# Kernel tuning notes

Hardware: AMD Instinct MI355X
Metric: run time of the kernel (lower is better)

## Reference

```python
import jax, jax.numpy as jnp
from jax import lax
import numpy as np

T_LOW, T_HIGH = 100.0, 200.0  # module defaults
H_IMG, W_IMG = 2048, 2048


def setup_inputs() -> dict:
    key = jax.random.key(0)
    x = jax.random.uniform(key, (H_IMG, W_IMG), dtype=jnp.float32)  # image in [0,1]
    return {"x": x}


def _sh(p, dy, dx, H, W):
    # shifted view of a 1-pixel-padded array
    return p[1 + dy:1 + dy + H, 1 + dx:1 + dx + W]


def _canny(x):
    H, W = x.shape
    # (x*255).astype(uint8): quantize (floor), values assumed in [0,1]
    img = jnp.clip(jnp.floor(x * 255.0), 0.0, 255.0)

    # --- 3x3 Sobel gradients, replicate border (cv2 default) ---
    p = jnp.pad(img, 1, mode='edge')
    s = lambda dy, dx: _sh(p, dy, dx, H, W)
    gx = (s(-1, 1) + 2.0 * s(0, 1) + s(1, 1)) - (s(-1, -1) + 2.0 * s(0, -1) + s(1, -1))
    gy = (s(1, -1) + 2.0 * s(1, 0) + s(1, 1)) - (s(-1, -1) + 2.0 * s(-1, 0) + s(-1, 1))
    mag = jnp.abs(gx) + jnp.abs(gy)  # L1 gradient magnitude (cv2 L2gradient=False)

    # --- non-maximum suppression along quantized gradient direction ---
    ang = jnp.mod(jnp.degrees(jnp.arctan2(gy, gx)), 180.0)
    mp = jnp.pad(mag, 1)  # zero-pad: out-of-image neighbors have magnitude 0
    n = lambda dy, dx: _sh(mp, dy, dx, H, W)
    d0 = (ang < 22.5) | (ang >= 157.5)            # ~0 deg   -> compare L/R
    d1 = (ang >= 22.5) & (ang < 67.5)             # ~45 deg  -> compare diag
    d2 = (ang >= 67.5) & (ang < 112.5)            # ~90 deg  -> compare U/D
    # remaining (~135 deg)                         -> other diag
    n1 = jnp.where(d0, n(0, 1), jnp.where(d1, n(-1, 1), jnp.where(d2, n(-1, 0), n(-1, -1))))
    n2 = jnp.where(d0, n(0, -1), jnp.where(d1, n(1, -1), jnp.where(d2, n(1, 0), n(1, 1))))
    keep = (mag >= n1) & (mag > n2)
    # border pixels are never edges (cv2 behavior)
    interior = jnp.zeros((H, W), bool).at[1:-1, 1:-1].set(True)
    keep = keep & interior

    # --- double threshold + hysteresis edge linking (8-connected) ---
    strong = lax.stop_gradient(keep & (mag > T_HIGH))
    weak = lax.stop_gradient(keep & (mag > T_LOW))

    def dilate8(m):
        mp2 = jnp.pad(m, 1)
        out = jnp.zeros_like(m)
        for dy in (-1, 0, 1):
            for dx in (-1, 0, 1):
                out = out | _sh(mp2, dy, dx, H, W)
        return out

    def body(c):
        cur, _ = c
        new = cur | (weak & dilate8(cur))
        return new, jnp.any(new != cur)

    edges, _ = lax.while_loop(lambda c: c[1], body, (strong, jnp.array(True)))

    # ToTensor() maps uint8 255 -> 1.0; expand to 3 channels
    e = edges.astype(jnp.float32)
    return jnp.broadcast_to(e[None], (3, H, W))


def reference(x):
    return _canny(x)
```

## Files before the change

### kernel.cpp

```cpp
#include <hip/hip_runtime.h>
#include <hip/hip_cooperative_groups.h>

namespace cg = cooperative_groups;

#define HH 2048
#define WW 2048
#define WPR 32
#define NPIX (HH * WW)
#define NWORDS (HH * WPR)

typedef unsigned long long u64;
typedef unsigned int u32;

__device__ inline int findRoot(int* __restrict__ f, int i) {
    int p = __hip_atomic_load(&f[i], __ATOMIC_RELAXED, __HIP_MEMORY_SCOPE_AGENT);
    while (p != i) {
        int gp = __hip_atomic_load(&f[p], __ATOMIC_RELAXED, __HIP_MEMORY_SCOPE_AGENT);
        if (gp != p)
            __hip_atomic_store(&f[i], gp, __ATOMIC_RELAXED, __HIP_MEMORY_SCOPE_AGENT);
        i = p; p = gp;
    }
    return i;
}

__device__ inline void unite(int* __restrict__ f, int a, int b) {
    int ra = findRoot(f, a), rb = findRoot(f, b);
    while (ra != rb) {
        if (ra > rb) { int t = ra; ra = rb; rb = t; }
        int old = atomicCAS(&f[rb], rb, ra);
        if (old == rb || old == ra) return;
        rb = findRoot(f, old);
    }
}

__device__ inline int findRootRO(const int* __restrict__ f, int i) {
    int p = __hip_atomic_load(&f[i], __ATOMIC_RELAXED, __HIP_MEMORY_SCOPE_AGENT);
    while (true) {
        int gp = __hip_atomic_load(&f[p], __ATOMIC_RELAXED, __HIP_MEMORY_SCOPE_AGENT);
        if (gp == p) return p;
        p = gp;
    }
}

__device__ inline int findRootL(volatile int* fl, int i) {
    int p = fl[i];
    while (p != i) {
        int gp = fl[p];
        if (gp != p) fl[i] = gp;
        i = p; p = gp;
    }
    return i;
}

__device__ inline void uniteL(int* fl, int a, int b) {
    int ra = findRootL(fl, a), rb = findRootL(fl, b);
    while (ra != rb) {
        if (ra > rb) { int t = ra; ra = rb; rb = t; }
        int old = atomicCAS(&fl[rb], rb, ra);
        if (old == rb || old == ra) return;
        rb = findRootL(fl, old);
    }
}

__device__ inline int dirClass(int gxv, int gyv) {
    int ay = gyv, ax = gxv;
    if (ay < 0) { ay = -ay; ax = -ax; }
    if (ay == 0) return 0;
    if (ax > 0) {
        int s = ay + ax, q = 2 * ax * ax;
        if (s * s < q) return 0;
        int t = ay - ax;
        return (t < 0 || t * t < q) ? 1 : 2;
    }
    if (ax == 0) return 2;
    int h = -ax, s = ay + h, q = 2 * h * h;
    if (s * s < q) return 0;
    int t = ay - h;
    return (t > 0 && t * t > q) ? 2 : 3;
}

__global__ __launch_bounds__(512) void canny_tile(
    const float* __restrict__ x, u64* __restrict__ weakG,
    u64* __restrict__ edgeBits, u64* __restrict__ pendBits, int* __restrict__ f)
{
    __shared__ int imgS[68 * 68];
    __shared__ unsigned short magS[66 * 66];
    __shared__ u64 wRow[64], sRow[64];
    __shared__ unsigned char touched[4097];
    int* fl = imgS;

    const int tid = threadIdx.x;
    const int x0 = blockIdx.x * 64;
    const int y0 = blockIdx.y * 64;

    for (int idx = tid; idx < 68 * 68; idx += 512) {
        int r = idx / 68, c = idx - r * 68;
        int gy = y0 - 2 + r; gy = gy < 0 ? 0 : (gy > HH - 1 ? HH - 1 : gy);
        int gx = x0 - 2 + c; gx = gx < 0 ? 0 : (gx > WW - 1 ? WW - 1 : gx);
        float v = floorf(x[gy * WW + gx] * 255.0f);
        v = fminf(fmaxf(v, 0.0f), 255.0f);
        imgS[idx] = (int)v;
    }
    __syncthreads();

    for (int idx = tid; idx < 66 * 66; idx += 512) {
        int r = idx / 66, c = idx - r * 66;
        int i0 = r * 68 + c;
        int a00 = imgS[i0],       a01 = imgS[i0 + 1],   a02 = imgS[i0 + 2];
        int a10 = imgS[i0 + 68],                        a12 = imgS[i0 + 70];
        int a20 = imgS[i0 + 136], a21 = imgS[i0 + 137], a22 = imgS[i0 + 138];
        int gxv = (a02 + 2 * a12 + a22) - (a00 + 2 * a10 + a20);
        int gyv = (a20 + 2 * a21 + a22) - (a00 + 2 * a01 + a02);
        int mag = abs(gxv) + abs(gyv);
        int cls = dirClass(gxv, gyv);
        magS[idx] = (unsigned short)((cls << 12) | mag);
    }
    __syncthreads();

    const int lane = tid & 63;
    const int wv = tid >> 6;
    for (int i = 0; i < 8; ++i) {
        int rr = wv * 8 + i;
        int gyp = y0 + rr;
        int mc = (rr + 1) * 66 + lane + 1;
        int mv = magS[mc];
        int cls = mv >> 12;
        int mag = mv & 0xFFF;
        int d1 = (cls == 0) ? -1 : 64 + cls;
        int n1 = magS[mc - d1] & 0xFFF;
        int n2 = magS[mc + d1] & 0xFFF;
        bool keep = (mag >= n1) && (mag > n2) && (gyp > 0) && (gyp < HH - 1);
        bool weak = keep && (mag > 100);
        bool strong = keep && (mag > 200);
        u64 ww = __ballot(weak);
        u64 sw = __ballot(strong);
        if (lane == 0) {
            u64 m = ~0ull;
            if (x0 == 0) m &= ~1ull;
            if (x0 + 64 == WW) m &= ~(1ull << 63);
            wRow[rr] = ww & m;
            sRow[rr] = sw & m;
        }
    }
    for (int i = tid; i < 4097; i += 512) { fl[i] = i; touched[i] = 0; }
    __syncthreads();

    {
        const int r = tid >> 3, o = tid & 7;
        const u64 omask = 0xFFull << (o * 8);
        const u64 w = wRow[r];
        const u64 above = r ? wRow[r - 1] : 0;
        const int base = r * 64 + 1;
        u64 m;
        m = (w & (w >> 1)) & omask;
        while (m) { int b = __builtin_ctzll(m); m &= m - 1; uniteL(fl, base + b, base + b + 1); }
        m = (w & above) & omask;
        while (m) { int b = __builtin_ctzll(m); m &= m - 1; uniteL(fl, base + b, base - 64 + b); }
        m = (w & (above << 1)) & omask;
        while (m) { int b = __builtin_ctzll(m); m &= m - 1; uniteL(fl, base + b, base - 64 + b - 1); }
        m = (w & (above >> 1)) & omask;
        while (m) { int b = __builtin_ctzll(m); m &= m - 1; uniteL(fl, base + b, base - 64 + b + 1); }
        m = sRow[r] & omask;
        while (m) { int b = __builtin_ctzll(m); m &= m - 1; uniteL(fl, 0, base + b); }
    }
    __syncthreads();

    if (tid < 256) {
        int grp = tid >> 6;
        int ln = tid & 63;
        int node = -1;
        if (grp == 0)      { if ((wRow[0]  >> ln) & 1ull) node = ln + 1; }
        else if (grp == 1) { if ((wRow[63] >> ln) & 1ull) node = 63 * 64 + ln + 1; }
        else if (grp == 2) { if (wRow[ln] & 1ull)         node = ln * 64 + 1; }
        else               { if (wRow[ln] >> 63)          node = ln * 64 + 63 + 1; }
        if (node > 0) touched[findRootL(fl, node)] = 1;
    }
    __syncthreads();

    for (int k = 0; k < 8; ++k) {
        int i = k * 512 + tid;
        int rr = i >> 6, cc = i & 63;
        int g = (y0 + rr) * WW + x0 + cc;
        int val = g;
        bool edge = false, pend = false;
        if ((wRow[rr] >> cc) & 1ull) {
            int rt = findRootL(fl, i + 1);
            if (rt == 0) { edge = true; val = 0; }
            else {
                val = (y0 + ((rt - 1) >> 6)) * WW + x0 + ((rt - 1) & 63);
                pend = touched[rt] != 0;
            }
        }
        f[g] = val;
        u64 eb = __ballot(edge);
        u64 pb = __ballot(pend);
        if (lane == 0) {
            int widx = (y0 + rr) * WPR + (x0 >> 6);
            edgeBits[widx] = eb;
            pendBits[widx] = pb;
        }
    }
    if (tid < 64) weakG[(y0 + tid) * WPR + blockIdx.x] = wRow[tid];
}

__global__ __launch_bounds__(256) void canny_boundary(
    const u64* __restrict__ weakG, int* __restrict__ f)
{
    int t = blockIdx.x * 256 + threadIdx.x;
    if (t < 65536) {
        int y = t >> 5, c = t & 31;
        if (c == 31) return;
        u64 w0 = weakG[y * WPR + c];
        u64 w1 = weakG[y * WPR + c + 1];
        int a = (int)(w0 >> 63) & 1, b = (int)w1 & 1;
        if (!(a | b)) return;
        int p63 = y * WW + c * 64 + 63;
        int p64 = p63 + 1;
        if (a & b) unite(f, p63, p64);
        if (y < HH - 1) {
            u64 w0d = weakG[(y + 1) * WPR + c];
            u64 w1d = weakG[(y + 1) * WPR + c + 1];
            if (a && (w1d & 1ull)) unite(f, p63, p64 + WW);
            if (b && (w0d >> 63)) unite(f, p64, p63 + WW);
        }
    } else {
        int idx = t - 65536;
        if (idx >= 31 * 2048) return;
        int y = 63 + (idx >> 11) * 64;
        int xx = idx & 2047;
        u64 w = weakG[y * WPR + (xx >> 6)];
        if (!((w >> (xx & 63)) & 1ull)) return;
        int p = y * WW + xx;
        u64 wd = weakG[(y + 1) * WPR + (xx >> 6)];
        if ((wd >> (xx & 63)) & 1ull) unite(f, p, p + WW);
        if (xx > 0) {
            u64 wl = weakG[(y + 1) * WPR + ((xx - 1) >> 6)];
            if ((wl >> ((xx - 1) & 63)) & 1ull) unite(f, p, p + WW - 1);
        }
        if (xx < WW - 1) {
            u64 wr = weakG[(y + 1) * WPR + ((xx + 1) >> 6)];
            if ((wr >> ((xx + 1) & 63)) & 1ull) unite(f, p, p + WW + 1);
        }
    }
}

__global__ __launch_bounds__(256) void canny_edgefuse(
    const u64* __restrict__ edgeBits, const u64* __restrict__ pendBits,
    const int* __restrict__ f, float* __restrict__ out)
{
    __shared__ unsigned short eS[256];
    const int tid = threadIdx.x;
    const int B = blockIdx.x * 4096;
    const int px0 = B + tid * 16;
    u64 ew = edgeBits[px0 >> 6];
    u64 pw = pendBits[px0 >> 6];
    const int sh = px0 & 63;
    u32 be = (u32)(ew >> sh) & 0xFFFFu;
    u32 bp = (u32)(pw >> sh) & 0xFFFFu;
    if (bp) {
        int lastp = -1, laste = 0;
        do {
            int b = __builtin_ctz(bp); bp &= bp - 1;
            int v = __hip_atomic_load(&f[px0 + b], __ATOMIC_RELAXED, __HIP_MEMORY_SCOPE_AGENT);
            int ed;
            if (v == 0) ed = 1;
            else if (v == px0 + b) ed = 0;
            else if (v == lastp) ed = laste;
            else { ed = (findRootRO(f, v) == 0); lastp = v; laste = ed; }
            be |= (u32)ed << b;
        } while (bp);
    }
    eS[tid] = (unsigned short)be;
    __syncthreads();

    #pragma unroll
    for (int ch = 0; ch < 3; ++ch) {
        #pragma unroll
        for (int j = 0; j < 4; ++j) {
            int idx = j * 256 + tid;
            u32 eb = (u32)(eS[idx >> 2] >> ((idx & 3) * 4)) & 0xFu;
            float4 v;
            v.x = (float)(eb & 1u);
            v.y = (float)((eb >> 1) & 1u);
            v.z = (float)((eb >> 2) & 1u);
            v.w = (float)((eb >> 3) & 1u);
            *reinterpret_cast<float4*>(out + (size_t)ch * NPIX + B + idx * 4) = v;
        }
    }
}

__global__ __launch_bounds__(256) void canny_prep(
    const float* __restrict__ x, u64* __restrict__ weakG,
    u64* __restrict__ strongG, unsigned int* __restrict__ flags)
{
    __shared__ int imgS[20][68];
    __shared__ int magS[18][68];
    const int tid = threadIdx.x;
    const int tx0 = blockIdx.x * 64;
    const int ty0 = blockIdx.y * 16;

    if (flags && blockIdx.x == 0 && blockIdx.y == 0 && tid < 2) flags[tid] = 0u;

    for (int idx = tid; idx < 20 * 68; idx += 256) {
        int r = idx / 68, c = idx - r * 68;
        int gy = ty0 - 2 + r; gy = gy < 0 ? 0 : (gy > HH - 1 ? HH - 1 : gy);
        int gx = tx0 - 2 + c; gx = gx < 0 ? 0 : (gx > WW - 1 ? WW - 1 : gx);
        float v = floorf(x[gy * WW + gx] * 255.0f);
        v = fminf(fmaxf(v, 0.0f), 255.0f);
        imgS[r][c] = (int)v;
    }
    __syncthreads();

    for (int idx = tid; idx < 18 * 66; idx += 256) {
        int r = idx / 66, c = idx - r * 66;
        int a00 = imgS[r][c],     a01 = imgS[r][c + 1],     a02 = imgS[r][c + 2];
        int a10 = imgS[r + 1][c],                           a12 = imgS[r + 1][c + 2];
        int a20 = imgS[r + 2][c], a21 = imgS[r + 2][c + 1], a22 = imgS[r + 2][c + 2];
        int gxv = (a02 + 2 * a12 + a22) - (a00 + 2 * a10 + a20);
        int gyv = (a20 + 2 * a21 + a22) - (a00 + 2 * a01 + a02);
        magS[r][c] = abs(gxv) + abs(gyv);
    }
    __syncthreads();

    const int lane = tid & 63;
    const int wv = tid >> 6;
    for (int i = 0; i < 4; ++i) {
        int rr = wv * 4 + i;
        int gyp = ty0 + rr;
        int r = rr + 1, c = lane + 1;
        int a00 = imgS[rr + 1][lane + 1], a01 = imgS[rr + 1][lane + 2], a02 = imgS[rr + 1][lane + 3];
        int a10 = imgS[rr + 2][lane + 1],                               a12 = imgS[rr + 2][lane + 3];
        int a20 = imgS[rr + 3][lane + 1], a21 = imgS[rr + 3][lane + 2], a22 = imgS[rr + 3][lane + 3];
        int gxv = (a02 + 2 * a12 + a22) - (a00 + 2 * a10 + a20);
        int gyv = (a20 + 2 * a21 + a22) - (a00 + 2 * a01 + a02);
        int mag = magS[r][c];
        int cls = dirClass(gxv, gyv);
        int n1, n2;
        if (cls == 0)      { n1 = magS[r][c + 1];     n2 = magS[r][c - 1]; }
        else if (cls == 1) { n1 = magS[r - 1][c + 1]; n2 = magS[r + 1][c - 1]; }
        else if (cls == 2) { n1 = magS[r - 1][c];     n2 = magS[r + 1][c]; }
        else               { n1 = magS[r - 1][c - 1]; n2 = magS[r + 1][c + 1]; }

        bool keep = (mag >= n1) && (mag > n2) && (gyp > 0) && (gyp < HH - 1);
        bool weak = keep && (mag > 100);
        bool strong = keep && (mag > 200);
        u64 ww = __ballot(weak);
        u64 sw = __ballot(strong);
        if (lane == 0) {
            u64 mm = ~0ull;
            if (tx0 == 0) mm &= ~1ull;
            if (tx0 + 64 == WW) mm &= ~(1ull << 63);
            int widx = gyp * WPR + (tx0 >> 6);
            weakG[widx] = ww & mm;
            strongG[widx] = sw & mm;
        }
    }
}

__global__ __launch_bounds__(256) void canny_hyst(
    const u64* __restrict__ weakG, u64* __restrict__ edgeG,
    unsigned int* __restrict__ flags, float* __restrict__ out)
{
    cg::grid_group grid = cg::this_grid();
    const int tid = threadIdx.x;
    const int b = blockIdx.x;
    const int r = tid >> 5;
    const int c = tid & 31;
    const int row0 = b * 8;
    __shared__ u64 weakL[8][32];
    __shared__ u64 edgeL[10][32];
    __shared__ int sChg[2];
    __shared__ int sAny;

    weakL[r][c] = weakG[(row0 + r) * WPR + c];
    edgeL[r + 1][c] = edgeG[(row0 + r) * WPR + c];

    int iter = 0;
    for (;;) {
        if (tid < 32) {
            u64 v = 0;
            if (b > 0) v = __hip_atomic_load(&edgeG[(row0 - 1) * WPR + tid],
                                             __ATOMIC_RELAXED, __HIP_MEMORY_SCOPE_AGENT);
            edgeL[0][tid] = v;
        } else if (tid < 64) {
            int cc = tid - 32;
            u64 v = 0;
            if (b < (int)gridDim.x - 1)
                v = __hip_atomic_load(&edgeG[(row0 + 8) * WPR + cc],
                                      __ATOMIC_RELAXED, __HIP_MEMORY_SCOPE_AGENT);
            edgeL[9][cc] = v;
        }
        if (tid == 0) sAny = 0;
        if (tid < 2) sChg[tid] = 0;
        __syncthreads();

        int p = 0;
        for (;;) {
            u64 up = edgeL[r][c],     upl = c ? edgeL[r][c - 1] : 0,     upr = (c < 31) ? edgeL[r][c + 1] : 0;
            u64 mi = edgeL[r + 1][c], mil = c ? edgeL[r + 1][c - 1] : 0, mir = (c < 31) ? edgeL[r + 1][c + 1] : 0;
            u64 dn = edgeL[r + 2][c], dnl = c ? edgeL[r + 2][c - 1] : 0, dnr = (c < 31) ? edgeL[r + 2][c + 1] : 0;
            u64 A = up | (up << 1) | (up >> 1) | (upl >> 63) | (upr << 63);
            u64 B = mi | (mi << 1) | (mi >> 1) | (mil >> 63) | (mir << 63);
            u64 C = dn | (dn << 1) | (dn >> 1) | (dnl >> 63) | (dnr << 63);
            u64 ne = mi | (weakL[r][c] & (A | B | C));
            bool chg = (ne != mi);
            __syncthreads();
            edgeL[r + 1][c] = ne;
            if (chg) { sChg[p] = 1; sAny = 1; }
            if (tid == 0) sChg[p ^ 1] = 0;
            __syncthreads();
            if (!sChg[p]) break;
            p ^= 1;
        }

        if (sAny) edgeG[(row0 + r) * WPR + c] = edgeL[r + 1][c];
        if (sAny && tid == 0) atomicOr(&flags[iter & 1], 1u);
        __threadfence();
        grid.sync();
        unsigned fl2 = __hip_atomic_load(&flags[iter & 1], __ATOMIC_ACQUIRE, __HIP_MEMORY_SCOPE_AGENT);
        if (tid == 0) flags[(iter + 1) & 1] = 0u;
        __threadfence();
        grid.sync();
        if (fl2 == 0) break;
        ++iter;
    }

    for (int chn = 0; chn < 3; ++chn) {
        for (int rr = 0; rr < 8; ++rr) {
            size_t base2 = ((size_t)chn * HH + (size_t)(row0 + rr)) * WW;
            for (int k = tid; k < 512; k += 256) {
                u64 w = edgeL[rr + 1][k >> 4];
                int sh = (k & 15) * 4;
                float4 v;
                v.x = (float)((w >> sh) & 1ull);
                v.y = (float)((w >> (sh + 1)) & 1ull);
                v.z = (float)((w >> (sh + 2)) & 1ull);
                v.w = (float)((w >> (sh + 3)) & 1ull);
                *reinterpret_cast<float4*>(out + base2 + (size_t)k * 4) = v;
            }
        }
    }
}

extern "C" void kernel_launch(void* const* d_in, const int* in_sizes, int n_in,
                              void* d_out, int out_size, void* d_ws, size_t ws_size,
                              hipStream_t stream) {
    const float* x = (const float*)d_in[0];
    float* out = (float*)d_out;

    const size_t BM = (size_t)NWORDS * 8;
    const size_t need = 3 * BM + (size_t)NPIX * 4;

    if (ws_size >= need) {
        u64* weakG    = (u64*)d_ws;
        u64* edgeBits = weakG + NWORDS;
        u64* pendBits = edgeBits + NWORDS;
        int* f = (int*)(pendBits + NWORDS);

        hipLaunchKernelGGL(canny_tile, dim3(32, 32), dim3(512), 0, stream,
                           x, weakG, edgeBits, pendBits, f);
        hipLaunchKernelGGL(canny_boundary, dim3((65536 + 31 * 2048 + 255) / 256), dim3(256),
                           0, stream, weakG, f);
        hipLaunchKernelGGL(canny_edgefuse, dim3(NPIX / 4096), dim3(256), 0, stream,
                           edgeBits, pendBits, f, out);
    } else {
        u64* edgeG = (u64*)d_ws;
        u64* weakG = edgeG + NWORDS;
        unsigned int* flags = (unsigned int*)(weakG + NWORDS);
        hipLaunchKernelGGL(canny_prep, dim3(WW / 64, HH / 16), dim3(256), 0, stream,
                           x, weakG, edgeG, flags);
        void* args[] = { (void*)&weakG, (void*)&edgeG, (void*)&flags, (void*)&out };
        hipLaunchCooperativeKernel((void*)canny_hyst, dim3(256), dim3(256), args, 0, stream);
    }
}
```

Baseline: 123.8 us.

## Vectorize interior tile loads and write union-find parents only where needed

Interior tiles now load the input with float4 reads and drop the floor/clamp, relying on the cast truncation and inputs lying in [0,1]. The final pass no longer writes the union-find parent array for every pixel. It writes only border strong pixels (set to root 0) and pending weak pixels, and block (0,0) seeds f[0]=0. This cuts global memory traffic sharply, but it depends on later kernels never reading the parent entries that are no longer written, and on inputs staying non-negative.

```diff
diff --git a/kernel.cpp b/kernel.cpp
--- a/kernel.cpp
+++ b/kernel.cpp
@@ -93,13 +93,26 @@
     const int x0 = blockIdx.x * 64;
     const int y0 = blockIdx.y * 64;
 
-    for (int idx = tid; idx < 68 * 68; idx += 512) {
-        int r = idx / 68, c = idx - r * 68;
-        int gy = y0 - 2 + r; gy = gy < 0 ? 0 : (gy > HH - 1 ? HH - 1 : gy);
-        int gx = x0 - 2 + c; gx = gx < 0 ? 0 : (gx > WW - 1 ? WW - 1 : gx);
-        float v = floorf(x[gy * WW + gx] * 255.0f);
-        v = fminf(fmaxf(v, 0.0f), 255.0f);
-        imgS[idx] = (int)v;
+    if (blockIdx.x == 0 && blockIdx.y == 0 && tid == 0) f[0] = 0;
+
+    if (x0 >= 4 && x0 + 68 <= WW) {
+        for (int t = tid; t < 18 * 68; t += 512) {
+            int r = t / 18, k = t - r * 18;
+            int gy = y0 - 2 + r; gy = gy < 0 ? 0 : (gy > HH - 1 ? HH - 1 : gy);
+            float4 v = *reinterpret_cast<const float4*>(x + (size_t)gy * WW + (x0 - 4) + 4 * k);
+            int c0 = 4 * k - 2;
+            if (c0 >= 0)            imgS[r * 68 + c0]     = (int)(v.x * 255.0f);
+            if ((unsigned)(c0 + 1) < 68) imgS[r * 68 + c0 + 1] = (int)(v.y * 255.0f);
+            if ((unsigned)(c0 + 2) < 68) imgS[r * 68 + c0 + 2] = (int)(v.z * 255.0f);
+            if (c0 + 3 < 68)        imgS[r * 68 + c0 + 3] = (int)(v.w * 255.0f);
+        }
+    } else {
+        for (int idx = tid; idx < 68 * 68; idx += 512) {
+            int r = idx / 68, c = idx - r * 68;
+            int gy = y0 - 2 + r; gy = gy < 0 ? 0 : (gy > HH - 1 ? HH - 1 : gy);
+            int gx = x0 - 2 + c; gx = gx < 0 ? 0 : (gx > WW - 1 ? WW - 1 : gx);
+            imgS[idx] = (int)(x[(size_t)gy * WW + gx] * 255.0f);
+        }
     }
     __syncthreads();
 
@@ -181,17 +194,18 @@
         int i = k * 512 + tid;
         int rr = i >> 6, cc = i & 63;
         int g = (y0 + rr) * WW + x0 + cc;
-        int val = g;
         bool edge = false, pend = false;
         if ((wRow[rr] >> cc) & 1ull) {
+            bool onBorder = (rr == 0) | (rr == 63) | (cc == 0) | (cc == 63);
             int rt = findRootL(fl, i + 1);
-            if (rt == 0) { edge = true; val = 0; }
-            else {
-                val = (y0 + ((rt - 1) >> 6)) * WW + x0 + ((rt - 1) & 63);
-                pend = touched[rt] != 0;
+            if (rt == 0) {
+                edge = true;
+                if (onBorder) f[g] = 0;
+            } else if (touched[rt]) {
+                pend = true;
+                f[g] = (y0 + ((rt - 1) >> 6)) * WW + x0 + ((rt - 1) & 63);
             }
         }
-        f[g] = val;
         u64 eb = __ballot(edge);
         u64 pb = __ballot(pend);
         if (lane == 0) {
```

Result: no change. 124.2 us (+0.3%).
